# Performance work log

Measured on AMD Instinct MI355X. Metric: run time of the kernel, lower is better.

## Reference

```python
import jax, jax.numpy as jnp
import numpy as np

NUM_CLASSES = 80
N_CAND = 10  # simOTA n_candidate_k


def setup_inputs() -> dict:
    key = jax.random.key(0)
    ks = jax.random.split(key, 8)
    G, C, B = 300, NUM_CLASSES, 2
    # FPN grids for a 1280x1280 input, strides 8/16/32 -> 160^2+80^2+40^2 = 33600 anchors
    levels = [(160, 8), (80, 16), (40, 32)]
    xs, ys, ss = [], [], []
    for n, s in levels:
        yy, xx = np.meshgrid(np.arange(n), np.arange(n), indexing='ij')
        xs.append(xx.ravel()); ys.append(yy.ravel()); ss.append(np.full(n * n, s))
    x_shifts = jnp.asarray(np.concatenate(xs), jnp.float32)[None]
    y_shifts = jnp.asarray(np.concatenate(ys), jnp.float32)[None]
    strides = jnp.asarray(np.concatenate(ss), jnp.float32)
    expanded_strides = strides[None]
    A = x_shifts.shape[1]
    # gt boxes in cxcywh, image coords
    gt_cxy = jax.random.uniform(ks[0], (G, 2), jnp.float32, 0.0, 1280.0)
    gt_wh = jax.random.uniform(ks[1], (G, 2), jnp.float32, 16.0, 256.0)
    gt_bboxes_per_image = jnp.concatenate([gt_cxy, gt_wh], -1)
    gt_classes = jax.random.randint(ks[2], (G,), 0, C)
    # predicted boxes: anchor centers + noise, wh ~ a few strides
    anc_x = (x_shifts[0] + 0.5) * strides
    anc_y = (y_shifts[0] + 0.5) * strides
    pr_cxy = jnp.stack([anc_x, anc_y], -1) + jax.random.normal(ks[3], (A, 2), jnp.float32) * strides[:, None]
    pr_wh = strides[:, None] * (1.0 + 4.0 * jax.random.uniform(ks[4], (A, 2), jnp.float32))
    bboxes_preds_per_image = jnp.concatenate([pr_cxy, pr_wh], -1)
    cls_preds = jax.random.normal(ks[5], (B, A, C), jnp.float32)
    obj_preds = jax.random.normal(ks[6], (B, A, 1), jnp.float32)
    return {
        'batch_idx': 0, 'num_gt': G, 'total_num_anchors': A,
        'gt_bboxes_per_image': gt_bboxes_per_image, 'gt_classes': gt_classes,
        'bboxes_preds_per_image': bboxes_preds_per_image,
        'expanded_strides': expanded_strides, 'x_shifts': x_shifts, 'y_shifts': y_shifts,
        'cls_preds': cls_preds, 'obj_preds': obj_preds,
    }


def _pairwise_iou(gt, pr):
    # gt [G,4], pr [A,4], cxcywh -> iou [G,A] (bboxes_iou with xyxy=False)
    tl = jnp.maximum(gt[:, None, :2] - 0.5 * gt[:, None, 2:], pr[None, :, :2] - 0.5 * pr[None, :, 2:])
    br = jnp.minimum(gt[:, None, :2] + 0.5 * gt[:, None, 2:], pr[None, :, :2] + 0.5 * pr[None, :, 2:])
    wh = jnp.clip(br - tl, 0.0)
    inter = wh[..., 0] * wh[..., 1]
    area_g = gt[:, 2] * gt[:, 3]
    area_p = pr[:, 2] * pr[:, 3]
    return inter / (area_g[:, None] + area_p[None, :] - inter)


def reference(batch_idx, num_gt, total_num_anchors, gt_bboxes_per_image, gt_classes,
              bboxes_preds_per_image, expanded_strides, x_shifts, y_shifts, cls_preds, obj_preds):
    G, A = gt_bboxes_per_image.shape[0], bboxes_preds_per_image.shape[0]
    strides = expanded_strides[0]
    xc = (x_shifts[0] + 0.5) * strides  # [A] anchor centers
    yc = (y_shifts[0] + 0.5) * strides
    gx, gy, gw, gh = (gt_bboxes_per_image[:, i] for i in range(4))
    # is_in_boxes [G,A]
    in_box = ((xc[None] > (gx - 0.5 * gw)[:, None]) & ((gx + 0.5 * gw)[:, None] > xc[None]) &
              (yc[None] > (gy - 0.5 * gh)[:, None]) & ((gy + 0.5 * gh)[:, None] > yc[None]))
    r = 2.5 * strides[None]  # center_radius * stride
    in_ctr = ((xc[None] > gx[:, None] - r) & (gx[:, None] + r > xc[None]) &
              (yc[None] > gy[:, None] - r) & (gy[:, None] + r > yc[None]))
    fg_any = in_box.any(0) | in_ctr.any(0)          # fg_mask over all anchors
    candidate = in_box & in_ctr                      # is_in_boxes_and_center (full-anchor layout)
    ious = jnp.where(fg_any[None, :], _pairwise_iou(gt_bboxes_per_image, bboxes_preds_per_image), 0.0)
    # pairwise cls BCE cost; one-hot target -> factored form, never materializes [G,A,C]
    p = jnp.sqrt(jax.nn.sigmoid(cls_preds[batch_idx]) * jax.nn.sigmoid(obj_preds[batch_idx]))  # [A,C]
    p = jnp.clip(p, 1e-7, 1.0 - 1e-7)
    lp, l1p = jnp.log(p), jnp.log1p(-p)
    s_all = l1p.sum(-1)                              # [A] sum_c log(1-p_c)
    cls_loss = -((lp - l1p)[:, gt_classes].T + s_all[None, :])  # [G,A]
    # cost; 1e5 penalty for non-candidates (as in source), extra 1e6 keeps non-fg anchors
    # strictly below any fg anchor in top-k order (source only ever considers fg anchors)
    cost = cls_loss - 3.0 * jnp.log(ious + 1e-8) + 100000.0 * (~candidate) + 1000000.0 * (~fg_any)[None, :]
    # dynamic-k: sum of top-10 ious per gt, clamped to >= 1 (<= 10 inherently)
    topk_ious, _ = jax.lax.top_k(ious, N_CAND)
    dks = jnp.clip(topk_ious.sum(1).astype(jnp.int32), 1, N_CAND)  # [G]
    _, idx = jax.lax.top_k(-cost, N_CAND)            # [G,10] lowest-cost anchors per gt
    sel = (jnp.arange(N_CAND)[None, :] < dks[:, None]).astype(jnp.int32)
    matching = jnp.zeros((G, A), jnp.int32).at[jnp.arange(G)[:, None], idx].max(sel)
    # resolve anchors matched to >1 gt: keep argmax of T_scores over gts (as in source)
    multi = matching.sum(0) > 1
    best_gt = jnp.argmax(cost, axis=0)               # [A]
    matching = jnp.where(multi[None, :], (jnp.arange(G)[:, None] == best_gt[None, :]).astype(jnp.int32), matching)
    fg_final = matching.sum(0) > 0                   # final fg mask over all anchors
    num_fg = fg_final.sum()
    matched = jnp.argmax(matching, axis=0)           # [A]
    gt_matched_classes = jnp.where(fg_final, gt_classes[matched], -1)
    pred_ious = (matching.astype(ious.dtype) * ious).sum(0)  # [A], 0 where unmatched
    matched_gt_inds = jnp.where(fg_final, matched, -1)
    # fixed-shape (full-anchor) versions of the source's compacted outputs
    return (gt_matched_classes, fg_final, pred_ious, matched_gt_inds, num_fg)
```

## Files before the change

### kernel.cpp

```cpp
#include <hip/hip_runtime.h>
#include <math.h>

#define NUMC 80
#define NCAND 10
#define NK 16
#define SEGI 16
#define SEGF 16
#define FBY  8
#define GT_LDS 300

typedef unsigned long long u64;

__device__ __forceinline__ float sigmoid_stable(float x) {
    float e = expf(-fabsf(x));
    float num = (x >= 0.0f) ? 1.0f : e;
    return num / (1.0f + e);
}

__device__ __forceinline__ float s_all_for(int a, int b, int A, float so,
                                           const float* __restrict__ cls)
{
    const float4* cp4 = (const float4*)(cls + ((size_t)b * A + a) * NUMC);
    float acc = 0.0f;
    for (int q = 0; q < NUMC/4; ++q) {
        float4 v4 = cp4[q];
        float vv[4] = {v4.x, v4.y, v4.z, v4.w};
        #pragma unroll
        for (int k = 0; k < 4; ++k) {
            float sc = sigmoid_stable(vv[k]);
            float p = sqrtf(sc * so);
            p = fminf(fmaxf(p, 1e-7f), 1.0f - 1e-7f);
            acc += log1pf(-p);
        }
    }
    return acc;
}

__device__ __forceinline__ void bitonic16_desc(float (&L)[NK]) {
    #pragma unroll
    for (int j = 0; j < NK; ++j) if (!(j & 8)) { float a=L[j], b=L[j|8]; L[j]=fmaxf(a,b); L[j|8]=fminf(a,b); }
    #pragma unroll
    for (int j = 0; j < NK; ++j) if (!(j & 4)) { float a=L[j], b=L[j|4]; L[j]=fmaxf(a,b); L[j|4]=fminf(a,b); }
    #pragma unroll
    for (int j = 0; j < NK; ++j) if (!(j & 2)) { float a=L[j], b=L[j|2]; L[j]=fmaxf(a,b); L[j|2]=fminf(a,b); }
    #pragma unroll
    for (int j = 0; j < NK; ++j) if (!(j & 1)) { float a=L[j], b=L[j|1]; L[j]=fmaxf(a,b); L[j|1]=fminf(a,b); }
}

__device__ __forceinline__ void merge16_desc(float (&A_)[NK], const float (&B_)[NK]) {
    float L[NK];
    #pragma unroll
    for (int j = 0; j < NK; ++j) L[j] = fmaxf(A_[j], B_[NK-1-j]);
    bitonic16_desc(L);
    #pragma unroll
    for (int j = 0; j < NK; ++j) A_[j] = L[j];
}

struct CostRes { float cost; float iou; bool cand; };

__device__ __forceinline__ CostRes cost_od(
    int g, int a, int b, int A,
    const float* __restrict__ gt, const float4* __restrict__ pred4,
    const float4* __restrict__ anc4, const float* __restrict__ s_arr,
    const float* __restrict__ so_arr, const float* __restrict__ cls,
    const int* __restrict__ fg_any, const int* __restrict__ gcls)
{
    float gx = gt[g*4+0], gy = gt[g*4+1], gw = gt[g*4+2], gh = gt[g*4+3];
    float4 p4 = pred4[a];
    float4 an = anc4[a];
    int fga = fg_any[a];
    float px = p4.x, py = p4.y, pw = p4.z, ph = p4.w;
    float tlx = fmaxf(gx - 0.5f*gw, px - 0.5f*pw);
    float tly = fmaxf(gy - 0.5f*gh, py - 0.5f*ph);
    float brx = fminf(gx + 0.5f*gw, px + 0.5f*pw);
    float bry = fminf(gy + 0.5f*gh, py + 0.5f*ph);
    float iw = fmaxf(brx - tlx, 0.0f);
    float ih = fmaxf(bry - tly, 0.0f);
    float inter = iw * ih;
    float iou = inter / (gw*gh + pw*ph - inter);
    float fi = fga ? iou : 0.0f;
    float x = an.x, y = an.y, r = an.z;
    bool inb = (x > gx - 0.5f*gw) && (gx + 0.5f*gw > x) &&
               (y > gy - 0.5f*gh) && (gy + 0.5f*gh > y);
    bool inc = (x > gx - r) && (gx + r > x) && (y > gy - r) && (gy + r > y);
    bool cand = inb && inc;
    float so = so_arr[a];
    float cv = cls[((size_t)b * A + a) * NUMC + gcls[g]];
    float sc = sigmoid_stable(cv);
    float p = sqrtf(sc * so);
    p = fminf(fmaxf(p, 1e-7f), 1.0f - 1e-7f);
    float lp = logf(p);
    float l1p = log1pf(-p);
    float clsl = -((lp - l1p) + s_arr[a]);
    float cost = clsl - 3.0f * logf(fi + 1e-8f)
               + (cand ? 0.0f : 100000.0f)
               + (fga  ? 0.0f : 1000000.0f);
    CostRes res; res.cost = cost; res.iou = fi; res.cand = cand; return res;
}

__device__ __forceinline__ float pair_iou_masked4(
    int g, const float* __restrict__ gt, float4 p4, int fga)
{
    float gx = gt[g*4+0], gy = gt[g*4+1], gw = gt[g*4+2], gh = gt[g*4+3];
    float px = p4.x, py = p4.y, pw = p4.z, ph = p4.w;
    float tlx = fmaxf(gx - 0.5f*gw, px - 0.5f*pw);
    float tly = fmaxf(gy - 0.5f*gh, py - 0.5f*ph);
    float brx = fminf(gx + 0.5f*gw, px + 0.5f*pw);
    float bry = fminf(gy + 0.5f*gh, py + 0.5f*ph);
    float iw = fmaxf(brx - tlx, 0.0f);
    float ih = fmaxf(bry - tly, 0.0f);
    float inter = iw * ih;
    float iou = inter / (gw*gh + pw*ph - inter);
    return fga ? iou : 0.0f;
}

__global__ __launch_bounds__(512) void fused_pre_kernel(
    const int* __restrict__ bidx, int G, int A,
    const float* __restrict__ gt, const float* __restrict__ strides,
    const float* __restrict__ xs, const float* __restrict__ ys,
    const float* __restrict__ obj, const float4* __restrict__ pred4,
    float4* __restrict__ anc4, float* __restrict__ so_arr, float* __restrict__ s_arr,
    float4* __restrict__ ptlbr4, float* __restrict__ pare, float4* __restrict__ grpbox,
    int* __restrict__ fg_any, int* __restrict__ cand_any,
    int* __restrict__ count, int* __restrict__ mgt,
    int* __restrict__ mcount, int* __restrict__ fb_cnt, float* __restrict__ out)
{
    __shared__ float sgt[GT_LDS * 4];
    __shared__ float sx[64], sy[64], sr[64];
    __shared__ int   flags[512];

    int tid = threadIdx.x;
    int a0 = blockIdx.x * 64;
    int GS = (G < GT_LDS) ? G : GT_LDS;

    for (int i = tid; i < GS * 4; i += 512) sgt[i] = gt[i];
    if (tid < 64) {
        int a = a0 + tid;
        float st = 0.0f, x = 0.0f, y = 0.0f;
        if (a < A) {
            st = strides[a];
            x = (xs[a] + 0.5f) * st;
            y = (ys[a] + 0.5f) * st;
            so_arr[a] = sigmoid_stable(obj[(size_t)bidx[0] * A + a]);
        }
        sx[tid] = x; sy[tid] = y; sr[tid] = 2.5f * st;
    }
    __syncthreads();

    {
        int a_loc = tid & 63;
        int chunk = tid >> 6;
        int a = a0 + a_loc;
        int any_or = 0, any_and = 0;
        if (a < A) {
            float x = sx[a_loc], y = sy[a_loc], r = sr[a_loc];
            int gpc = (G + 7) >> 3;
            int g0 = chunk * gpc;
            int g1 = min(G, g0 + gpc);
            for (int g = g0; g < g1; ++g) {
                float gx, gy, gw, gh;
                if (g < GS) { gx = sgt[g*4+0]; gy = sgt[g*4+1]; gw = sgt[g*4+2]; gh = sgt[g*4+3]; }
                else        { gx = gt[g*4+0];  gy = gt[g*4+1];  gw = gt[g*4+2];  gh = gt[g*4+3]; }
                bool inb = (x > gx - 0.5f*gw) && (gx + 0.5f*gw > x) &&
                           (y > gy - 0.5f*gh) && (gy + 0.5f*gh > y);
                bool inc = (x > gx - r) && (gx + r > x) && (y > gy - r) && (gy + r > y);
                any_or  |= (int)(inb | inc);
                any_and |= (int)(inb && inc);
            }
        }
        flags[tid] = any_or | (any_and << 1);
    }
    __syncthreads();

    if (tid < 64) {
        int a = a0 + tid;
        float mnx = INFINITY, mny = INFINITY, mxx = -INFINITY, mxy = -INFINITY;
        if (a < A) {
            int f = flags[tid] | flags[tid+64] | flags[tid+128] | flags[tid+192]
                  | flags[tid+256] | flags[tid+320] | flags[tid+384] | flags[tid+448];
            int any = f & 1;
            fg_any[a] = any;
            cand_any[a] = (f >> 1) & 1;
            anc4[a] = make_float4(sx[tid], sy[tid], sr[tid], 0.0f);
            s_arr[a] = 0.0f;
            count[a] = 0;
            mgt[a] = -1;
            float4 p4 = pred4[a];
            pare[a] = p4.z * p4.w;
            if (any) {
                mnx = p4.x - 0.5f * p4.z;
                mny = p4.y - 0.5f * p4.w;
                mxx = p4.x + 0.5f * p4.z;
                mxy = p4.y + 0.5f * p4.w;
            }
            ptlbr4[a] = make_float4(mnx, mny, mxx, mxy);
        }
        #pragma unroll
        for (int off = 32; off > 0; off >>= 1) {
            mnx = fminf(mnx, __shfl_xor(mnx, off));
            mny = fminf(mny, __shfl_xor(mny, off));
            mxx = fmaxf(mxx, __shfl_xor(mxx, off));
            mxy = fmaxf(mxy, __shfl_xor(mxy, off));
        }
        if (tid == 0) {
            grpbox[blockIdx.x] = make_float4(mnx, mny, mxx, mxy);
            if (blockIdx.x == 0) { out[(size_t)4 * A] = 0.0f; mcount[0] = 0; fb_cnt[0] = 0; }
        }
    }
}

__global__ void sall_kernel(
    const int* __restrict__ bidx, int A,
    const float* __restrict__ cls, const float* __restrict__ so_arr,
    const int* __restrict__ cand_any, float* __restrict__ s_arr)
{
    int a = blockIdx.x * blockDim.x + threadIdx.x;
    if (a >= A) return;
    if (!cand_any[a]) return;
    s_arr[a] = s_all_for(a, bidx[0], A, so_arr[a], cls);
}

__global__ void sall_fixup_kernel(
    const int* __restrict__ bidx, int A,
    const float* __restrict__ cls, const float* __restrict__ so_arr,
    const int* __restrict__ cand_any, const int* __restrict__ fb_cnt,
    float* __restrict__ s_arr)
{
    if (fb_cnt[0] == 0) return;
    int a = blockIdx.x * blockDim.x + threadIdx.x;
    if (a >= A) return;
    if (cand_any[a]) return;
    s_arr[a] = s_all_for(a, bidx[0], A, so_arr[a], cls);
}

__global__ __launch_bounds__(64) void scanI_kernel(
    int G, int A, int seglen,
    const float* __restrict__ gt,
    const float4* __restrict__ ptlbr4, const float* __restrict__ pare,
    const float4* __restrict__ grpbox,
    float* __restrict__ piou_ws)
{
    int seg = blockIdx.x;
    int g = blockIdx.y;
    int a0 = seg * seglen;
    int a1 = min(A, a0 + seglen);
    int tid = threadIdx.x;

    float gx = gt[g*4+0], gy = gt[g*4+1], gw = gt[g*4+2], gh = gt[g*4+3];
    float gtlx = gx - 0.5f*gw, gtly = gy - 0.5f*gh;
    float gbrx = gx + 0.5f*gw, gbry = gy + 0.5f*gh;
    float ag = gw * gh;

    float ti[NK];
    #pragma unroll
    for (int j = 0; j < NK; ++j) ti[j] = 0.0f;

    for (int a = a0 + tid; a < a1; a += 64) {
        int grp = __builtin_amdgcn_readfirstlane(a >> 6);
        float4 gb = grpbox[grp];
        if ((gb.z <= gtlx) || (gb.x >= gbrx) || (gb.w <= gtly) || (gb.y >= gbry))
            continue;
        float4 p = ptlbr4[a];
        float ap = pare[a];
        float tlx = fmaxf(gtlx, p.x);
        float tly = fmaxf(gtly, p.y);
        float brx = fminf(gbrx, p.z);
        float bry = fminf(gbry, p.w);
        float iw = fmaxf(brx - tlx, 0.0f);
        float ih = fmaxf(bry - tly, 0.0f);
        float inter = iw * ih;
        float fi = inter / (ag + ap - inter);
        if (fi > ti[NK-1]) {
            ti[NK-1] = fi;
            #pragma unroll
            for (int j = NK-1; j >= 1; --j) {
                if (ti[j] > ti[j-1]) { float t = ti[j]; ti[j] = ti[j-1]; ti[j-1] = t; }
            }
        }
    }

    #pragma unroll
    for (int lv = 0; lv < 6; ++lv) {
        int off = 1 << lv;
        float pv[NK];
        #pragma unroll
        for (int j = 0; j < NK; ++j) pv[j] = __shfl_xor(ti[j], off);
        merge16_desc(ti, pv);
    }
    if (tid == 0) {
        int base = (g * SEGI + seg) * NCAND;
        #pragma unroll
        for (int j = 0; j < NCAND; ++j) piou_ws[base + j] = ti[j];
    }
}

__global__ __launch_bounds__(256) void scanC_kernel(
    const int* __restrict__ bidx, int G, int A,
    const float* __restrict__ gt, const float4* __restrict__ pred4,
    const float4* __restrict__ anc4, const float* __restrict__ s_arr,
    const float* __restrict__ so_arr, const float* __restrict__ cls,
    const int* __restrict__ fg_any, const int* __restrict__ gcls,
    const float* __restrict__ piou_ws,
    int* __restrict__ dk_arr, int* __restrict__ fb_list, int* __restrict__ fb_cnt,
    int* __restrict__ count, int* __restrict__ mgt)
{
    int g = blockIdx.x;
    int tid = threadIdx.x;
    __shared__ u64 scand[128];
    __shared__ int s_nc;
    __shared__ int s_dk;

    if (tid == 0) s_nc = 0;
    if (tid < 64) {
        float acc[NK];
        const float* ib = piou_ws + ((size_t)g * SEGI + (tid < SEGI ? tid : 0)) * NCAND;
        #pragma unroll
        for (int j = 0; j < NK; ++j)
            acc[j] = (j < NCAND && tid < SEGI) ? ib[j] : 0.0f;
        #pragma unroll
        for (int lv = 0; lv < 4; ++lv) {
            int off = 1 << lv;
            float pv[NK];
            #pragma unroll
            for (int j = 0; j < NK; ++j) pv[j] = __shfl_xor(acc[j], off);
            merge16_desc(acc, pv);
        }
        if (tid == 0) {
            float s = 0.0f;
            #pragma unroll
            for (int j = 0; j < NCAND; ++j) s += acc[j];
            int dk = (int)s;
            if (dk < 1) dk = 1;
            if (dk > NCAND) dk = NCAND;
            s_dk = dk;
            dk_arr[g] = dk;
        }
    }
    __syncthreads();

    if (tid < 243) {
        int lvl = tid / 81, slot = tid % 81, sxi = slot % 9, syi = slot / 9;
        int n, si, base;
        if (lvl == 0)      { n = 160; si = 8;  base = 0; }
        else if (lvl == 1) { n = 80;  si = 16; base = 25600; }
        else               { n = 40;  si = 32; base = 32000; }
        float sf = (float)si;
        float gx = gt[g*4+0], gy = gt[g*4+1], gw = gt[g*4+2], gh = gt[g*4+3];
        float mx = fminf(0.5f*gw, 2.5f*sf);
        float my = fminf(0.5f*gh, 2.5f*sf);
        int ilo = (int)floorf((gx - mx)/sf - 0.5f) - 1;
        int ihi = (int)ceilf ((gx + mx)/sf - 0.5f) + 1;
        int jlo = (int)floorf((gy - my)/sf - 0.5f) - 1;
        int jhi = (int)ceilf ((gy + my)/sf - 0.5f) + 1;
        if (ilo < 0) ilo = 0;
        if (jlo < 0) jlo = 0;
        if (ihi > n-1) ihi = n-1;
        if (jhi > n-1) jhi = n-1;
        int i = ilo + sxi, j = jlo + syi;
        if (i <= ihi && j <= jhi) {
            int a = base + j * n + i;
            int b = bidx[0];
            CostRes cr = cost_od(g, a, b, A, gt, pred4, anc4, s_arr, so_arr, cls, fg_any, gcls);
            if (cr.cand) {
                int k = atomicAdd(&s_nc, 1);
                if (k < 128)
                    scand[k] = ((u64)__float_as_uint(cr.cost) << 32) | (unsigned)a;
            }
        }
    }
    __syncthreads();

    if (tid == 0) {
        int nc = s_nc; if (nc > 128) nc = 128;
        int dk = s_dk;
        if (dk > nc) {
            int idx = atomicAdd(fb_cnt, 1);
            fb_list[idx] = g;
        } else {
            u64 top[NCAND];
            #pragma unroll
            for (int j = 0; j < NCAND; ++j) top[j] = ~0ULL;
            for (int t = 0; t < nc; ++t) {
                u64 v = scand[t];
                if (v < top[NCAND-1]) {
                    top[NCAND-1] = v;
                    #pragma unroll
                    for (int j = NCAND-1; j >= 1; --j) {
                        if (top[j] < top[j-1]) { u64 t2 = top[j]; top[j] = top[j-1]; top[j-1] = t2; }
                    }
                }
            }
            #pragma unroll
            for (int o = 0; o < NCAND; ++o) {
                if (o < dk) {
                    int a = (int)(top[o] & 0xffffffffULL);
                    atomicAdd(&count[a], 1);
                    atomicMax(&mgt[a], g);
                }
            }
        }
    }
}

__global__ __launch_bounds__(256) void fb_part_kernel(
    const int* __restrict__ bidx, int G, int A, int seglenF,
    const float* __restrict__ gt, const float4* __restrict__ pred4,
    const float4* __restrict__ anc4, const float* __restrict__ s_arr,
    const float* __restrict__ so_arr, const float* __restrict__ cls,
    const int* __restrict__ fg_any, const int* __restrict__ gcls,
    const int* __restrict__ fb_list, const int* __restrict__ fb_cnt,
    u64* __restrict__ fbws)
{
    __shared__ u64 s_cv[256 * NCAND];
    int nflag = fb_cnt[0];
    int tid = threadIdx.x;
    int chunk = blockIdx.x;
    int b = bidx[0];
    for (int f = blockIdx.y; f < nflag; f += FBY) {
        int g = fb_list[f];
        int a0 = chunk * seglenF;
        int a1 = min(A, a0 + seglenF);
        u64 tc[NCAND];
        #pragma unroll
        for (int j = 0; j < NCAND; ++j) tc[j] = ~0ULL;
        for (int a = a0 + tid; a < a1; a += 256) {
            CostRes cr = cost_od(g, a, b, A, gt, pred4, anc4, s_arr, so_arr, cls, fg_any, gcls);
            u64 v = ((u64)__float_as_uint(cr.cost) << 32) | (unsigned)a;
            if (v < tc[NCAND-1]) {
                tc[NCAND-1] = v;
                #pragma unroll
                for (int j = NCAND-1; j >= 1; --j) {
                    if (tc[j] < tc[j-1]) { u64 t2 = tc[j]; tc[j] = tc[j-1]; tc[j-1] = t2; }
                }
            }
        }
        #pragma unroll
        for (int j = 0; j < NCAND; ++j) s_cv[tid*NCAND+j] = tc[j];
        __syncthreads();
        for (int off = 128; off > 0; off >>= 1) {
            if (tid < off) {
                u64 rc[NCAND];
                int i = 0, k = 0;
                const u64* L = &s_cv[tid*NCAND];
                const u64* R = &s_cv[(tid+off)*NCAND];
                for (int o = 0; o < NCAND; ++o) {
                    if (L[i] < R[k]) { rc[o] = L[i]; ++i; }
                    else             { rc[o] = R[k]; ++k; }
                }
                for (int j = 0; j < NCAND; ++j) s_cv[tid*NCAND+j] = rc[j];
            }
            __syncthreads();
        }
        if (tid == 0) {
            u64* dst = fbws + ((size_t)f * SEGF + chunk) * NCAND;
            for (int j = 0; j < NCAND; ++j) dst[j] = s_cv[j];
        }
        __syncthreads();
    }
}

__global__ void fb_mark_kernel(
    const int* __restrict__ fb_list, const int* __restrict__ fb_cnt,
    const int* __restrict__ dk_arr, const u64* __restrict__ fbws,
    int* __restrict__ count, int* __restrict__ mgt)
{
    if (threadIdx.x != 0 || blockIdx.x != 0) return;
    int nflag = fb_cnt[0];
    for (int f = 0; f < nflag; ++f) {
        int g = fb_list[f];
        int dk = dk_arr[g];
        const u64* lists = fbws + (size_t)f * SEGF * NCAND;
        int p[SEGF];
        for (int q = 0; q < SEGF; ++q) p[q] = 0;
        for (int o = 0; o < dk; ++o) {
            int bs = 0; u64 bv = ~0ULL;
            for (int q = 0; q < SEGF; ++q) {
                if (p[q] < NCAND) {
                    u64 v = lists[q*NCAND + p[q]];
                    if (v < bv) { bv = v; bs = q; }
                }
            }
            p[bs]++;
            int a = (int)(bv & 0xffffffffULL);
            atomicAdd(&count[a], 1);
            atomicMax(&mgt[a], g);
        }
    }
}

__global__ void finalize_a_kernel(
    int G, int A,
    const float* __restrict__ gt, const float4* __restrict__ pred4,
    const int* __restrict__ fg_any, const int* __restrict__ gcls,
    const int* __restrict__ count, const int* __restrict__ mgt,
    int* __restrict__ mlist, int* __restrict__ mcount,
    float* __restrict__ out)
{
    int a = blockIdx.x * blockDim.x + threadIdx.x;
    if (a >= A) return;
    int cnt = count[a];
    unsigned long long m = __ballot(cnt > 0);
    if ((threadIdx.x & 63) == 0 && m) {
        atomicAdd(&out[(size_t)4*A], (float)__popcll(m));
    }
    if (cnt > 1) {
        int idx = atomicAdd(mcount, 1);
        mlist[idx] = a;
        out[(size_t)A + a] = 1.0f;
        return;
    }
    float gmc = -1.0f, mgi = -1.0f, piou = 0.0f, fg = 0.0f;
    if (cnt == 1) {
        int matched = mgt[a];
        fg = 1.0f;
        gmc = (float)gcls[matched];
        mgi = (float)matched;
        piou = pair_iou_masked4(matched, gt, pred4[a], fg_any[a]);
    }
    out[a]               = gmc;
    out[(size_t)A + a]   = fg;
    out[(size_t)2*A + a] = piou;
    out[(size_t)3*A + a] = mgi;
}

__global__ __launch_bounds__(256) void finalize_b_kernel(
    const int* __restrict__ bidx, int G, int A,
    const float* __restrict__ gt, const float4* __restrict__ pred4,
    const float4* __restrict__ anc4, const float* __restrict__ s_arr,
    const float* __restrict__ so_arr, const float* __restrict__ cls,
    const int* __restrict__ fg_any, const int* __restrict__ gcls,
    const int* __restrict__ mlist, const int* __restrict__ mcount,
    float* __restrict__ out)
{
    __shared__ float sc[256];
    __shared__ int   sg[256];
    int n = mcount[0];
    int tid = threadIdx.x;
    int b = bidx[0];
    for (int i = blockIdx.x; i < n; i += gridDim.x) {
        int a = mlist[i];
        float best = -INFINITY; int bi = 0x7fffffff;
        for (int g = tid; g < G; g += 256) {
            CostRes cr = cost_od(g, a, b, A, gt, pred4, anc4, s_arr, so_arr, cls, fg_any, gcls);
            if (cr.cost > best) { best = cr.cost; bi = g; }
        }
        sc[tid] = best; sg[tid] = bi;
        __syncthreads();
        for (int off = 128; off > 0; off >>= 1) {
            if (tid < off) {
                float c2 = sc[tid+off]; int g2 = sg[tid+off];
                if (c2 > sc[tid] || (c2 == sc[tid] && g2 < sg[tid])) { sc[tid] = c2; sg[tid] = g2; }
            }
            __syncthreads();
        }
        if (tid == 0) {
            int matched = sg[0];
            out[a]               = (float)gcls[matched];
            out[(size_t)2*A + a] = pair_iou_masked4(matched, gt, pred4[a], fg_any[a]);
            out[(size_t)3*A + a] = (float)matched;
        }
        __syncthreads();
    }
}

extern "C" void kernel_launch(void* const* d_in, const int* in_sizes, int n_in,
                              void* d_out, int out_size, void* d_ws, size_t ws_size,
                              hipStream_t stream)
{
    const int*   bidx    = (const int*)d_in[0];
    const float* gt      = (const float*)d_in[3];
    const int*   gcls    = (const int*)d_in[4];
    const float* pred    = (const float*)d_in[5];
    const float* strides = (const float*)d_in[6];
    const float* xs      = (const float*)d_in[7];
    const float* ys      = (const float*)d_in[8];
    const float* cls     = (const float*)d_in[9];
    const float* obj     = (const float*)d_in[10];
    int G = in_sizes[4];
    int A = in_sizes[6];
    float* out = (float*)d_out;
    const float4* pred4 = (const float4*)pred;

    char* ws = (char*)d_ws;
    size_t off = 0;
    auto alloc = [&](size_t bytes) -> void* {
        void* p = ws + off;
        off += (bytes + 255) & ~(size_t)255;
        return p;
    };
    int nGrp = (A + 63) / 64;
    float4* anc4     = (float4*)alloc((size_t)A * sizeof(float4));
    float*  so_arr   = (float*) alloc((size_t)A * sizeof(float));
    float*  s_arr    = (float*) alloc((size_t)A * sizeof(float));
    float4* ptlbr4   = (float4*)alloc((size_t)A * sizeof(float4));
    float*  pare     = (float*) alloc((size_t)A * sizeof(float));
    float4* grpbox   = (float4*)alloc((size_t)nGrp * sizeof(float4));
    int*    fg_any   = (int*)   alloc((size_t)A * sizeof(int));
    int*    cand_any = (int*)   alloc((size_t)A * sizeof(int));
    int*    count    = (int*)   alloc((size_t)A * sizeof(int));
    int*    mgt      = (int*)   alloc((size_t)A * sizeof(int));
    int*    mlist    = (int*)   alloc((size_t)A * sizeof(int));
    int*    mcount   = (int*)   alloc(256);
    int*    fb_cnt   = (int*)   alloc(256);
    float*  piou_ws  = (float*) alloc((size_t)G * SEGI * NCAND * sizeof(float));
    int*    dk_arr   = (int*)   alloc((size_t)G * sizeof(int));
    int*    fb_list  = (int*)   alloc((size_t)G * sizeof(int));
    u64*    fbws     = (u64*)   alloc((size_t)G * SEGF * NCAND * sizeof(u64));

    int seglenI = ((A + SEGI*64 - 1) / (SEGI*64)) * 64;
    int seglenF = ((A + SEGF*64 - 1) / (SEGF*64)) * 64;
    int blocksA256 = (A + 255) / 256;

    fused_pre_kernel<<<nGrp, 512, 0, stream>>>(
        bidx, G, A, gt, strides, xs, ys, obj, pred4,
        anc4, so_arr, s_arr, ptlbr4, pare, grpbox,
        fg_any, cand_any, count, mgt, mcount, fb_cnt, out);
    sall_kernel<<<blocksA256, 256, 0, stream>>>(
        bidx, A, cls, so_arr, cand_any, s_arr);
    scanI_kernel<<<dim3(SEGI, G), 64, 0, stream>>>(
        G, A, seglenI, gt, ptlbr4, pare, grpbox, piou_ws);
    scanC_kernel<<<G, 256, 0, stream>>>(
        bidx, G, A, gt, pred4, anc4, s_arr, so_arr, cls, fg_any, gcls,
        piou_ws, dk_arr, fb_list, fb_cnt, count, mgt);
    sall_fixup_kernel<<<blocksA256, 256, 0, stream>>>(
        bidx, A, cls, so_arr, cand_any, fb_cnt, s_arr);
    fb_part_kernel<<<dim3(SEGF, FBY), 256, 0, stream>>>(
        bidx, G, A, seglenF, gt, pred4, anc4, s_arr, so_arr, cls, fg_any, gcls,
        fb_list, fb_cnt, fbws);
    fb_mark_kernel<<<1, 64, 0, stream>>>(
        fb_list, fb_cnt, dk_arr, fbws, count, mgt);
    finalize_a_kernel<<<blocksA256, 256, 0, stream>>>(
        G, A, gt, pred4, fg_any, gcls, count, mgt, mlist, mcount, out);
    finalize_b_kernel<<<256, 256, 0, stream>>>(
        bidx, G, A, gt, pred4, anc4, s_arr, so_arr, cls, fg_any, gcls,
        mlist, mcount, out);
}
```

Before: 182.2 us.

## Fuse the simOTA kernel chain into one cooperative persistent kernel with grid syncs

Replaces the chain of nine kernel launches with a single cooperative kernel of 256 blocks that runs the phases in sequence, separated by grid-wide syncs. The per-anchor class log-sum is computed cooperatively inside the pre-pass, with eight threads per anchor writing partial terms to shared memory. The segmented top-k IoU scan and its workspace are replaced by per-gt processing inside the fused kernel, and the fallback and finalize steps now live in the same kernel with wave-level argmax reductions. This removes launch gaps and intermediate global round-trips, at the cost of grid-sync overhead and a fixed grid of 256 blocks, which limits parallelism in the per-gt phase.

Result: slower. 333.8 us (+83.2%).

```diff
diff --git a/kernel.cpp b/kernel.cpp
--- a/kernel.cpp
+++ b/kernel.cpp
@@ -1,59 +1,33 @@
 #include <hip/hip_runtime.h>
+#include <hip/hip_cooperative_groups.h>
 #include <math.h>
+
+namespace cg = cooperative_groups;
 
 #define NUMC 80
 #define NCAND 10
-#define NK 16
-#define SEGI 16
-#define SEGF 16
-#define FBY  8
+#define NB 256
+#define NT 512
 #define GT_LDS 300
 
 typedef unsigned long long u64;
+
+#define OFF_SGT 0
+#define OFF_L1P 4800
+#define OFF_FLG 25536
+#define OFF_XYR 27584
+#define OFF_IV  0
+#define OFF_SCD 20480
+#define OFF_MSC 21504
+#define OFF_CV  0
+#define OFF_ML  0
+#define OFF_MC  2048
+#define SMEM_BYTES 28352
 
 __device__ __forceinline__ float sigmoid_stable(float x) {
     float e = expf(-fabsf(x));
     float num = (x >= 0.0f) ? 1.0f : e;
     return num / (1.0f + e);
-}
-
-__device__ __forceinline__ float s_all_for(int a, int b, int A, float so,
-                                           const float* __restrict__ cls)
-{
-    const float4* cp4 = (const float4*)(cls + ((size_t)b * A + a) * NUMC);
-    float acc = 0.0f;
-    for (int q = 0; q < NUMC/4; ++q) {
-        float4 v4 = cp4[q];
-        float vv[4] = {v4.x, v4.y, v4.z, v4.w};
-        #pragma unroll
-        for (int k = 0; k < 4; ++k) {
-            float sc = sigmoid_stable(vv[k]);
-            float p = sqrtf(sc * so);
-            p = fminf(fmaxf(p, 1e-7f), 1.0f - 1e-7f);
-            acc += log1pf(-p);
-        }
-    }
-    return acc;
-}
-
-__device__ __forceinline__ void bitonic16_desc(float (&L)[NK]) {
-    #pragma unroll
-    for (int j = 0; j < NK; ++j) if (!(j & 8)) { float a=L[j], b=L[j|8]; L[j]=fmaxf(a,b); L[j|8]=fminf(a,b); }
-    #pragma unroll
-    for (int j = 0; j < NK; ++j) if (!(j & 4)) { float a=L[j], b=L[j|4]; L[j]=fmaxf(a,b); L[j|4]=fminf(a,b); }
-    #pragma unroll
-    for (int j = 0; j < NK; ++j) if (!(j & 2)) { float a=L[j], b=L[j|2]; L[j]=fmaxf(a,b); L[j|2]=fminf(a,b); }
-    #pragma unroll
-    for (int j = 0; j < NK; ++j) if (!(j & 1)) { float a=L[j], b=L[j|1]; L[j]=fmaxf(a,b); L[j|1]=fminf(a,b); }
-}
-
-__device__ __forceinline__ void merge16_desc(float (&A_)[NK], const float (&B_)[NK]) {
-    float L[NK];
-    #pragma unroll
-    for (int j = 0; j < NK; ++j) L[j] = fmaxf(A_[j], B_[NK-1-j]);
-    bitonic16_desc(L);
-    #pragma unroll
-    for (int j = 0; j < NK; ++j) A_[j] = L[j];
 }
 
 struct CostRes { float cost; float iou; bool cand; };
@@ -114,452 +88,419 @@
     return fga ? iou : 0.0f;
 }
 
-__global__ __launch_bounds__(512) void fused_pre_kernel(
+__global__ __launch_bounds__(NT, 4) void simota_all(
     const int* __restrict__ bidx, int G, int A,
-    const float* __restrict__ gt, const float* __restrict__ strides,
+    const float* __restrict__ gt, const int* __restrict__ gcls,
+    const float4* __restrict__ pred4, const float* __restrict__ strides,
     const float* __restrict__ xs, const float* __restrict__ ys,
-    const float* __restrict__ obj, const float4* __restrict__ pred4,
+    const float* __restrict__ cls, const float* __restrict__ obj,
     float4* __restrict__ anc4, float* __restrict__ so_arr, float* __restrict__ s_arr,
     float4* __restrict__ ptlbr4, float* __restrict__ pare, float4* __restrict__ grpbox,
     int* __restrict__ fg_any, int* __restrict__ cand_any,
     int* __restrict__ count, int* __restrict__ mgt,
-    int* __restrict__ mcount, int* __restrict__ fb_cnt, float* __restrict__ out)
+    int* __restrict__ dk_arr, int* __restrict__ fb_list, int* __restrict__ fb_cnt,
+    float* __restrict__ out)
 {
-    __shared__ float sgt[GT_LDS * 4];
-    __shared__ float sx[64], sy[64], sr[64];
-    __shared__ int   flags[512];
+    cg::grid_group grid = cg::this_grid();
+    __shared__ __align__(16) char smem[SMEM_BYTES];
 
     int tid = threadIdx.x;
-    int a0 = blockIdx.x * 64;
+    int bid = blockIdx.x;
+    int b = bidx[0];
     int GS = (G < GT_LDS) ? G : GT_LDS;
-
-    for (int i = tid; i < GS * 4; i += 512) sgt[i] = gt[i];
-    if (tid < 64) {
-        int a = a0 + tid;
-        float st = 0.0f, x = 0.0f, y = 0.0f;
-        if (a < A) {
-            st = strides[a];
-            x = (xs[a] + 0.5f) * st;
-            y = (ys[a] + 0.5f) * st;
-            so_arr[a] = sigmoid_stable(obj[(size_t)bidx[0] * A + a]);
-        }
-        sx[tid] = x; sy[tid] = y; sr[tid] = 2.5f * st;
+    int nGrp = (A + 63) >> 6;
+
+    {
+        float* sgt = (float*)(smem + OFF_SGT);
+        float* sl1p = (float*)(smem + OFF_L1P);
+        int*   sflg = (int*)(smem + OFF_FLG);
+        float* sx = (float*)(smem + OFF_XYR);
+        float* sy = sx + 64;
+        float* sr = sy + 64;
+
+        for (int i = tid; i < GS * 4; i += NT) sgt[i] = gt[i];
+        __syncthreads();
+
+        for (int grp = bid; grp < nGrp; grp += NB) {
+            int a0 = grp << 6;
+            if (tid < 64) {
+                int a = a0 + tid;
+                float st = 0.0f, x = 0.0f, y = 0.0f;
+                if (a < A) {
+                    st = strides[a];
+                    x = (xs[a] + 0.5f) * st;
+                    y = (ys[a] + 0.5f) * st;
+                    so_arr[a] = sigmoid_stable(obj[(size_t)b * A + a]);
+                }
+                sx[tid] = x; sy[tid] = y; sr[tid] = 2.5f * st;
+            }
+            __syncthreads();
+            {
+                int a_loc = tid & 63, chunk = tid >> 6;
+                int a = a0 + a_loc;
+                int any_or = 0, any_and = 0;
+                if (a < A) {
+                    float x = sx[a_loc], y = sy[a_loc], r = sr[a_loc];
+                    int gpc = (G + 7) >> 3;
+                    int g0 = chunk * gpc;
+                    int g1 = min(G, g0 + gpc);
+                    for (int g = g0; g < g1; ++g) {
+                        float gx, gy, gw, gh;
+                        if (g < GS) { gx = sgt[g*4+0]; gy = sgt[g*4+1]; gw = sgt[g*4+2]; gh = sgt[g*4+3]; }
+                        else        { gx = gt[g*4+0];  gy = gt[g*4+1];  gw = gt[g*4+2];  gh = gt[g*4+3]; }
+                        bool inb = (x > gx - 0.5f*gw) && (gx + 0.5f*gw > x) &&
+                                   (y > gy - 0.5f*gh) && (gy + 0.5f*gh > y);
+                        bool inc = (x > gx - r) && (gx + r > x) && (y > gy - r) && (gy + r > y);
+                        any_or  |= (int)(inb | inc);
+                        any_and |= (int)(inb && inc);
+                    }
+                }
+                sflg[tid] = any_or | (any_and << 1);
+            }
+            __syncthreads();
+            if (tid < 64) {
+                int a = a0 + tid;
+                float mnx = INFINITY, mny = INFINITY, mxx = -INFINITY, mxy = -INFINITY;
+                int f = sflg[tid] | sflg[tid+64] | sflg[tid+128] | sflg[tid+192]
+                      | sflg[tid+256] | sflg[tid+320] | sflg[tid+384] | sflg[tid+448];
+                int fg = f & 1, cd = (f >> 1) & 1;
+                if (a < A) {
+                    fg_any[a] = fg;
+                    cand_any[a] = cd;
+                    anc4[a] = make_float4(sx[tid], sy[tid], sr[tid], 0.0f);
+                    count[a] = 0;
+                    mgt[a] = -1;
+                    float4 p4 = pred4[a];
+                    pare[a] = p4.z * p4.w;
+                    if (fg) {
+                        mnx = p4.x - 0.5f * p4.z;
+                        mny = p4.y - 0.5f * p4.w;
+                        mxx = p4.x + 0.5f * p4.z;
+                        mxy = p4.y + 0.5f * p4.w;
+                    }
+                    ptlbr4[a] = make_float4(mnx, mny, mxx, mxy);
+                }
+                #pragma unroll
+                for (int off = 32; off > 0; off >>= 1) {
+                    mnx = fminf(mnx, __shfl_xor(mnx, off));
+                    mny = fminf(mny, __shfl_xor(mny, off));
+                    mxx = fmaxf(mxx, __shfl_xor(mxx, off));
+                    mxy = fmaxf(mxy, __shfl_xor(mxy, off));
+                }
+                if (tid == 0) grpbox[grp] = make_float4(mnx, mny, mxx, mxy);
+                sflg[tid] = cd;
+            }
+            __syncthreads();
+            {
+                int a_loc = tid >> 3, part = tid & 7;
+                int a = a0 + a_loc;
+                if (a < A && sflg[a_loc]) {
+                    float so = so_arr[a];
+                    const float* cp = cls + ((size_t)b * A + a) * NUMC + part * 10;
+                    #pragma unroll
+                    for (int j = 0; j < 10; ++j) {
+                        float sc = sigmoid_stable(cp[j]);
+                        float p = sqrtf(sc * so);
+                        p = fminf(fmaxf(p, 1e-7f), 1.0f - 1e-7f);
+                        sl1p[a_loc * 81 + part * 10 + j] = log1pf(-p);
+                    }
+                }
+            }
+            __syncthreads();
+            if (tid < 64) {
+                int a = a0 + tid;
+                if (a < A) {
+                    if (sflg[tid]) {
+                        float acc = 0.0f;
+                        #pragma unroll 8
+                        for (int c = 0; c < NUMC; ++c) acc += sl1p[tid * 81 + c];
+                        s_arr[a] = acc;
+                    } else {
+                        s_arr[a] = 0.0f;
+                    }
+                }
+            }
+            __syncthreads();
+        }
+        if (bid == 0 && tid == 0) { out[(size_t)4 * A] = 0.0f; fb_cnt[0] = 0; }
     }
-    __syncthreads();
+    grid.sync();
 
     {
-        int a_loc = tid & 63;
-        int chunk = tid >> 6;
-        int a = a0 + a_loc;
-        int any_or = 0, any_and = 0;
-        if (a < A) {
-            float x = sx[a_loc], y = sy[a_loc], r = sr[a_loc];
-            int gpc = (G + 7) >> 3;
-            int g0 = chunk * gpc;
-            int g1 = min(G, g0 + gpc);
-            for (int g = g0; g < g1; ++g) {
-                float gx, gy, gw, gh;
-                if (g < GS) { gx = sgt[g*4+0]; gy = sgt[g*4+1]; gw = sgt[g*4+2]; gh = sgt[g*4+3]; }
-                else        { gx = gt[g*4+0];  gy = gt[g*4+1];  gw = gt[g*4+2];  gh = gt[g*4+3]; }
-                bool inb = (x > gx - 0.5f*gw) && (gx + 0.5f*gw > x) &&
-                           (y > gy - 0.5f*gh) && (gy + 0.5f*gh > y);
-                bool inc = (x > gx - r) && (gx + r > x) && (y > gy - r) && (gy + r > y);
-                any_or  |= (int)(inb | inc);
-                any_and |= (int)(inb && inc);
-            }
-        }
-        flags[tid] = any_or | (any_and << 1);
-    }
-    __syncthreads();
-
-    if (tid < 64) {
-        int a = a0 + tid;
-        float mnx = INFINITY, mny = INFINITY, mxx = -INFINITY, mxy = -INFINITY;
-        if (a < A) {
-            int f = flags[tid] | flags[tid+64] | flags[tid+128] | flags[tid+192]
-                  | flags[tid+256] | flags[tid+320] | flags[tid+384] | flags[tid+448];
-            int any = f & 1;
-            fg_any[a] = any;
-            cand_any[a] = (f >> 1) & 1;
-            anc4[a] = make_float4(sx[tid], sy[tid], sr[tid], 0.0f);
-            s_arr[a] = 0.0f;
-            count[a] = 0;
-            mgt[a] = -1;
-            float4 p4 = pred4[a];
-            pare[a] = p4.z * p4.w;
-            if (any) {
-                mnx = p4.x - 0.5f * p4.z;
-                mny = p4.y - 0.5f * p4.w;
-                mxx = p4.x + 0.5f * p4.z;
-                mxy = p4.y + 0.5f * p4.w;
-            }
-            ptlbr4[a] = make_float4(mnx, mny, mxx, mxy);
-        }
-        #pragma unroll
-        for (int off = 32; off > 0; off >>= 1) {
-            mnx = fminf(mnx, __shfl_xor(mnx, off));
-            mny = fminf(mny, __shfl_xor(mny, off));
-            mxx = fmaxf(mxx, __shfl_xor(mxx, off));
-            mxy = fmaxf(mxy, __shfl_xor(mxy, off));
-        }
-        if (tid == 0) {
-            grpbox[blockIdx.x] = make_float4(mnx, mny, mxx, mxy);
-            if (blockIdx.x == 0) { out[(size_t)4 * A] = 0.0f; mcount[0] = 0; fb_cnt[0] = 0; }
-        }
-    }
-}
-
-__global__ void sall_kernel(
-    const int* __restrict__ bidx, int A,
-    const float* __restrict__ cls, const float* __restrict__ so_arr,
-    const int* __restrict__ cand_any, float* __restrict__ s_arr)
-{
-    int a = blockIdx.x * blockDim.x + threadIdx.x;
-    if (a >= A) return;
-    if (!cand_any[a]) return;
-    s_arr[a] = s_all_for(a, bidx[0], A, so_arr[a], cls);
-}
-
-__global__ void sall_fixup_kernel(
-    const int* __restrict__ bidx, int A,
-    const float* __restrict__ cls, const float* __restrict__ so_arr,
-    const int* __restrict__ cand_any, const int* __restrict__ fb_cnt,
-    float* __restrict__ s_arr)
-{
-    if (fb_cnt[0] == 0) return;
-    int a = blockIdx.x * blockDim.x + threadIdx.x;
-    if (a >= A) return;
-    if (cand_any[a]) return;
-    s_arr[a] = s_all_for(a, bidx[0], A, so_arr[a], cls);
-}
-
-__global__ __launch_bounds__(64) void scanI_kernel(
-    int G, int A, int seglen,
-    const float* __restrict__ gt,
-    const float4* __restrict__ ptlbr4, const float* __restrict__ pare,
-    const float4* __restrict__ grpbox,
-    float* __restrict__ piou_ws)
-{
-    int seg = blockIdx.x;
-    int g = blockIdx.y;
-    int a0 = seg * seglen;
-    int a1 = min(A, a0 + seglen);
-    int tid = threadIdx.x;
-
-    float gx = gt[g*4+0], gy = gt[g*4+1], gw = gt[g*4+2], gh = gt[g*4+3];
-    float gtlx = gx - 0.5f*gw, gtly = gy - 0.5f*gh;
-    float gbrx = gx + 0.5f*gw, gbry = gy + 0.5f*gh;
-    float ag = gw * gh;
-
-    float ti[NK];
-    #pragma unroll
-    for (int j = 0; j < NK; ++j) ti[j] = 0.0f;
-
-    for (int a = a0 + tid; a < a1; a += 64) {
-        int grp = __builtin_amdgcn_readfirstlane(a >> 6);
-        float4 gb = grpbox[grp];
-        if ((gb.z <= gtlx) || (gb.x >= gbrx) || (gb.w <= gtly) || (gb.y >= gbry))
-            continue;
-        float4 p = ptlbr4[a];
-        float ap = pare[a];
-        float tlx = fmaxf(gtlx, p.x);
-        float tly = fmaxf(gtly, p.y);
-        float brx = fminf(gbrx, p.z);
-        float bry = fminf(gbry, p.w);
-        float iw = fmaxf(brx - tlx, 0.0f);
-        float ih = fmaxf(bry - tly, 0.0f);
-        float inter = iw * ih;
-        float fi = inter / (ag + ap - inter);
-        if (fi > ti[NK-1]) {
-            ti[NK-1] = fi;
+        float* s_iv = (float*)(smem + OFF_IV);
+        u64*   scand = (u64*)(smem + OFF_SCD);
+        int*   smisc = (int*)(smem + OFF_MSC);
+
+        for (int g = bid; g < G; g += NB) {
+            float gx = gt[g*4+0], gy = gt[g*4+1], gw = gt[g*4+2], gh = gt[g*4+3];
+            float gtlx = gx - 0.5f*gw, gtly = gy - 0.5f*gh;
+            float gbrx = gx + 0.5f*gw, gbry = gy + 0.5f*gh;
+            float ag = gw * gh;
+
+            float ti[NCAND];
             #pragma unroll
-            for (int j = NK-1; j >= 1; --j) {
-                if (ti[j] > ti[j-1]) { float t = ti[j]; ti[j] = ti[j-1]; ti[j-1] = t; }
-            }
-        }
-    }
-
-    #pragma unroll
-    for (int lv = 0; lv < 6; ++lv) {
-        int off = 1 << lv;
-        float pv[NK];
-        #pragma unroll
-        for (int j = 0; j < NK; ++j) pv[j] = __shfl_xor(ti[j], off);
-        merge16_desc(ti, pv);
-    }
-    if (tid == 0) {
-        int base = (g * SEGI + seg) * NCAND;
-        #pragma unroll
-        for (int j = 0; j < NCAND; ++j) piou_ws[base + j] = ti[j];
-    }
-}
-
-__global__ __launch_bounds__(256) void scanC_kernel(
-    const int* __restrict__ bidx, int G, int A,
-    const float* __restrict__ gt, const float4* __restrict__ pred4,
-    const float4* __restrict__ anc4, const float* __restrict__ s_arr,
-    const float* __restrict__ so_arr, const float* __restrict__ cls,
-    const int* __restrict__ fg_any, const int* __restrict__ gcls,
-    const float* __restrict__ piou_ws,
-    int* __restrict__ dk_arr, int* __restrict__ fb_list, int* __restrict__ fb_cnt,
-    int* __restrict__ count, int* __restrict__ mgt)
-{
-    int g = blockIdx.x;
-    int tid = threadIdx.x;
-    __shared__ u64 scand[128];
-    __shared__ int s_nc;
-    __shared__ int s_dk;
-
-    if (tid == 0) s_nc = 0;
-    if (tid < 64) {
-        float acc[NK];
-        const float* ib = piou_ws + ((size_t)g * SEGI + (tid < SEGI ? tid : 0)) * NCAND;
-        #pragma unroll
-        for (int j = 0; j < NK; ++j)
-            acc[j] = (j < NCAND && tid < SEGI) ? ib[j] : 0.0f;
-        #pragma unroll
-        for (int lv = 0; lv < 4; ++lv) {
-            int off = 1 << lv;
-            float pv[NK];
-            #pragma unroll
-            for (int j = 0; j < NK; ++j) pv[j] = __shfl_xor(acc[j], off);
-            merge16_desc(acc, pv);
-        }
-        if (tid == 0) {
-            float s = 0.0f;
-            #pragma unroll
-            for (int j = 0; j < NCAND; ++j) s += acc[j];
-            int dk = (int)s;
-            if (dk < 1) dk = 1;
-            if (dk > NCAND) dk = NCAND;
-            s_dk = dk;
-            dk_arr[g] = dk;
-        }
-    }
-    __syncthreads();
-
-    if (tid < 243) {
-        int lvl = tid / 81, slot = tid % 81, sxi = slot % 9, syi = slot / 9;
-        int n, si, base;
-        if (lvl == 0)      { n = 160; si = 8;  base = 0; }
-        else if (lvl == 1) { n = 80;  si = 16; base = 25600; }
-        else               { n = 40;  si = 32; base = 32000; }
-        float sf = (float)si;
-        float gx = gt[g*4+0], gy = gt[g*4+1], gw = gt[g*4+2], gh = gt[g*4+3];
-        float mx = fminf(0.5f*gw, 2.5f*sf);
-        float my = fminf(0.5f*gh, 2.5f*sf);
-        int ilo = (int)floorf((gx - mx)/sf - 0.5f) - 1;
-        int ihi = (int)ceilf ((gx + mx)/sf - 0.5f) + 1;
-        int jlo = (int)floorf((gy - my)/sf - 0.5f) - 1;
-        int jhi = (int)ceilf ((gy + my)/sf - 0.5f) + 1;
-        if (ilo < 0) ilo = 0;
-        if (jlo < 0) jlo = 0;
-        if (ihi > n-1) ihi = n-1;
-        if (jhi > n-1) jhi = n-1;
-        int i = ilo + sxi, j = jlo + syi;
-        if (i <= ihi && j <= jhi) {
-            int a = base + j * n + i;
-            int b = bidx[0];
-            CostRes cr = cost_od(g, a, b, A, gt, pred4, anc4, s_arr, so_arr, cls, fg_any, gcls);
-            if (cr.cand) {
-                int k = atomicAdd(&s_nc, 1);
-                if (k < 128)
-                    scand[k] = ((u64)__float_as_uint(cr.cost) << 32) | (unsigned)a;
-            }
-        }
-    }
-    __syncthreads();
-
-    if (tid == 0) {
-        int nc = s_nc; if (nc > 128) nc = 128;
-        int dk = s_dk;
-        if (dk > nc) {
-            int idx = atomicAdd(fb_cnt, 1);
-            fb_list[idx] = g;
-        } else {
-            u64 top[NCAND];
-            #pragma unroll
-            for (int j = 0; j < NCAND; ++j) top[j] = ~0ULL;
-            for (int t = 0; t < nc; ++t) {
-                u64 v = scand[t];
-                if (v < top[NCAND-1]) {
-                    top[NCAND-1] = v;
+            for (int j = 0; j < NCAND; ++j) ti[j] = 0.0f;
+
+            for (int a = tid; a < A; a += NT) {
+                int grp = __builtin_amdgcn_readfirstlane(a >> 6);
+                float4 gb = grpbox[grp];
+                if ((gb.z <= gtlx) || (gb.x >= gbrx) || (gb.w <= gtly) || (gb.y >= gbry))
+                    continue;
+                float4 p = ptlbr4[a];
+                float ap = pare[a];
+                float tlx = fmaxf(gtlx, p.x);
+                float tly = fmaxf(gtly, p.y);
+                float brx = fminf(gbrx, p.z);
+                float bry = fminf(gbry, p.w);
+                float iw = fmaxf(brx - tlx, 0.0f);
+                float ih = fmaxf(bry - tly, 0.0f);
+                float inter = iw * ih;
+                float fi = inter / (ag + ap - inter);
+                if (fi > ti[NCAND-1]) {
+                    ti[NCAND-1] = fi;
                     #pragma unroll
                     for (int j = NCAND-1; j >= 1; --j) {
-                        if (top[j] < top[j-1]) { u64 t2 = top[j]; top[j] = top[j-1]; top[j-1] = t2; }
+                        if (ti[j] > ti[j-1]) { float t = ti[j]; ti[j] = ti[j-1]; ti[j-1] = t; }
                     }
                 }
             }
             #pragma unroll
-            for (int o = 0; o < NCAND; ++o) {
-                if (o < dk) {
-                    int a = (int)(top[o] & 0xffffffffULL);
+            for (int j = 0; j < NCAND; ++j) s_iv[tid*NCAND+j] = ti[j];
+            __syncthreads();
+            for (int off = NT/2; off > 0; off >>= 1) {
+                if (tid < off) {
+                    float ra[NCAND];
+                    int i = 0, k = 0;
+                    const float* L = &s_iv[tid*NCAND];
+                    const float* R = &s_iv[(tid+off)*NCAND];
+                    for (int o = 0; o < NCAND; ++o) {
+                        if (L[i] >= R[k]) { ra[o] = L[i]; ++i; }
+                        else              { ra[o] = R[k]; ++k; }
+                    }
+                    for (int j = 0; j < NCAND; ++j) s_iv[tid*NCAND+j] = ra[j];
+                }
+                __syncthreads();
+            }
+            if (tid == 0) {
+                float s = 0.0f;
+                #pragma unroll
+                for (int j = 0; j < NCAND; ++j) s += s_iv[j];
+                int dk = (int)s;
+                if (dk < 1) dk = 1;
+                if (dk > NCAND) dk = NCAND;
+                smisc[0] = 0;
+                smisc[1] = dk;
+                dk_arr[g] = dk;
+            }
+            __syncthreads();
+            if (tid < 243) {
+                int lvl = tid / 81, slot = tid % 81, sxi = slot % 9, syi = slot / 9;
+                int n, si, base;
+                if (lvl == 0)      { n = 160; si = 8;  base = 0; }
+                else if (lvl == 1) { n = 80;  si = 16; base = 25600; }
+                else               { n = 40;  si = 32; base = 32000; }
+                float sf = (float)si;
+                float mx = fminf(0.5f*gw, 2.5f*sf);
+                float my = fminf(0.5f*gh, 2.5f*sf);
+                int ilo = (int)floorf((gx - mx)/sf - 0.5f) - 1;
+                int ihi = (int)ceilf ((gx + mx)/sf - 0.5f) + 1;
+                int jlo = (int)floorf((gy - my)/sf - 0.5f) - 1;
+                int jhi = (int)ceilf ((gy + my)/sf - 0.5f) + 1;
+                if (ilo < 0) ilo = 0;
+                if (jlo < 0) jlo = 0;
+                if (ihi > n-1) ihi = n-1;
+                if (jhi > n-1) jhi = n-1;
+                int i = ilo + sxi, j = jlo + syi;
+                if (i <= ihi && j <= jhi) {
+                    int a = base + j * n + i;
+                    CostRes cr = cost_od(g, a, b, A, gt, pred4, anc4, s_arr, so_arr, cls, fg_any, gcls);
+                    if (cr.cand) {
+                        int k = atomicAdd(&smisc[0], 1);
+                        if (k < 128)
+                            scand[k] = ((u64)__float_as_uint(cr.cost) << 32) | (unsigned)a;
+                    }
+                }
+            }
+            __syncthreads();
+            if (tid == 0) {
+                int nc = smisc[0]; if (nc > 128) nc = 128;
+                int dk = smisc[1];
+                if (dk > nc) {
+                    int idx = atomicAdd(fb_cnt, 1);
+                    fb_list[idx] = g;
+                } else {
+                    u64 top[NCAND];
+                    #pragma unroll
+                    for (int j = 0; j < NCAND; ++j) top[j] = ~0ULL;
+                    for (int t = 0; t < nc; ++t) {
+                        u64 v = scand[t];
+                        if (v < top[NCAND-1]) {
+                            top[NCAND-1] = v;
+                            #pragma unroll
+                            for (int j = NCAND-1; j >= 1; --j) {
+                                if (top[j] < top[j-1]) { u64 t2 = top[j]; top[j] = top[j-1]; top[j-1] = t2; }
+                            }
+                        }
+                    }
+                    #pragma unroll
+                    for (int o = 0; o < NCAND; ++o) {
+                        if (o < dk) {
+                            int a = (int)(top[o] & 0xffffffffULL);
+                            atomicAdd(&count[a], 1);
+                            atomicMax(&mgt[a], g);
+                        }
+                    }
+                }
+            }
+            __syncthreads();
+        }
+    }
+    grid.sync();
+
+    int nfb = fb_cnt[0];
+    if (nfb > 0) {
+        float* sl1p = (float*)(smem + OFF_L1P);
+        int*   sflg = (int*)(smem + OFF_FLG);
+        for (int grp = bid; grp < nGrp; grp += NB) {
+            int a0 = grp << 6;
+            if (tid < 64) {
+                int a = a0 + tid;
+                sflg[tid] = (a < A) ? cand_any[a] : 1;
+            }
+            __syncthreads();
+            {
+                int a_loc = tid >> 3, part = tid & 7;
+                int a = a0 + a_loc;
+                if (a < A && !sflg[a_loc]) {
+                    float so = so_arr[a];
+                    const float* cp = cls + ((size_t)b * A + a) * NUMC + part * 10;
+                    #pragma unroll
+                    for (int j = 0; j < 10; ++j) {
+                        float sc = sigmoid_stable(cp[j]);
+                        float p = sqrtf(sc * so);
+                        p = fminf(fmaxf(p, 1e-7f), 1.0f - 1e-7f);
+                        sl1p[a_loc * 81 + part * 10 + j] = log1pf(-p);
+                    }
+                }
+            }
+            __syncthreads();
+            if (tid < 64) {
+                int a = a0 + tid;
+                if (a < A && !sflg[tid]) {
+                    float acc = 0.0f;
+                    #pragma unroll 8
+                    for (int c = 0; c < NUMC; ++c) acc += sl1p[tid * 81 + c];
+                    s_arr[a] = acc;
+                }
+            }
+            __syncthreads();
+        }
+    }
+    grid.sync();
+
+    if (nfb > 0) {
+        u64* s_cv = (u64*)(smem + OFF_CV);
+        for (int f = bid; f < nfb; f += NB) {
+            int g = fb_list[f];
+            int dk = dk_arr[g];
+            if (tid < 256) {
+                u64 tc[NCAND];
+                #pragma unroll
+                for (int j = 0; j < NCAND; ++j) tc[j] = ~0ULL;
+                for (int a = tid; a < A; a += 256) {
+                    CostRes cr = cost_od(g, a, b, A, gt, pred4, anc4, s_arr, so_arr, cls, fg_any, gcls);
+                    u64 v = ((u64)__float_as_uint(cr.cost) << 32) | (unsigned)a;
+                    if (v < tc[NCAND-1]) {
+                        tc[NCAND-1] = v;
+                        #pragma unroll
+                        for (int j = NCAND-1; j >= 1; --j) {
+                            if (tc[j] < tc[j-1]) { u64 t2 = tc[j]; tc[j] = tc[j-1]; tc[j-1] = t2; }
+                        }
+                    }
+                }
+                #pragma unroll
+                for (int j = 0; j < NCAND; ++j) s_cv[tid*NCAND+j] = tc[j];
+            }
+            __syncthreads();
+            for (int off = 128; off > 0; off >>= 1) {
+                if (tid < off) {
+                    u64 rc[NCAND];
+                    int i = 0, k = 0;
+                    const u64* L = &s_cv[tid*NCAND];
+                    const u64* R = &s_cv[(tid+off)*NCAND];
+                    for (int o = 0; o < NCAND; ++o) {
+                        if (L[i] < R[k]) { rc[o] = L[i]; ++i; }
+                        else             { rc[o] = R[k]; ++k; }
+                    }
+                    for (int j = 0; j < NCAND; ++j) s_cv[tid*NCAND+j] = rc[j];
+                }
+                __syncthreads();
+            }
+            if (tid == 0) {
+                for (int o = 0; o < dk; ++o) {
+                    int a = (int)(s_cv[o] & 0xffffffffULL);
                     atomicAdd(&count[a], 1);
                     atomicMax(&mgt[a], g);
                 }
             }
+            __syncthreads();
         }
     }
-}
-
-__global__ __launch_bounds__(256) void fb_part_kernel(
-    const int* __restrict__ bidx, int G, int A, int seglenF,
-    const float* __restrict__ gt, const float4* __restrict__ pred4,
-    const float4* __restrict__ anc4, const float* __restrict__ s_arr,
-    const float* __restrict__ so_arr, const float* __restrict__ cls,
-    const int* __restrict__ fg_any, const int* __restrict__ gcls,
-    const int* __restrict__ fb_list, const int* __restrict__ fb_cnt,
-    u64* __restrict__ fbws)
-{
-    __shared__ u64 s_cv[256 * NCAND];
-    int nflag = fb_cnt[0];
-    int tid = threadIdx.x;
-    int chunk = blockIdx.x;
-    int b = bidx[0];
-    for (int f = blockIdx.y; f < nflag; f += FBY) {
-        int g = fb_list[f];
-        int a0 = chunk * seglenF;
-        int a1 = min(A, a0 + seglenF);
-        u64 tc[NCAND];
-        #pragma unroll
-        for (int j = 0; j < NCAND; ++j) tc[j] = ~0ULL;
-        for (int a = a0 + tid; a < a1; a += 256) {
-            CostRes cr = cost_od(g, a, b, A, gt, pred4, anc4, s_arr, so_arr, cls, fg_any, gcls);
-            u64 v = ((u64)__float_as_uint(cr.cost) << 32) | (unsigned)a;
-            if (v < tc[NCAND-1]) {
-                tc[NCAND-1] = v;
-                #pragma unroll
-                for (int j = NCAND-1; j >= 1; --j) {
-                    if (tc[j] < tc[j-1]) { u64 t2 = tc[j]; tc[j] = tc[j-1]; tc[j-1] = t2; }
-                }
-            }
-        }
-        #pragma unroll
-        for (int j = 0; j < NCAND; ++j) s_cv[tid*NCAND+j] = tc[j];
+    grid.sync();
+
+    {
+        int* mlist = (int*)(smem + OFF_ML);
+        int* mcnt  = (int*)(smem + OFF_MC);
+        if (tid == 0) mcnt[0] = 0;
         __syncthreads();
-        for (int off = 128; off > 0; off >>= 1) {
-            if (tid < off) {
-                u64 rc[NCAND];
-                int i = 0, k = 0;
-                const u64* L = &s_cv[tid*NCAND];
-                const u64* R = &s_cv[(tid+off)*NCAND];
-                for (int o = 0; o < NCAND; ++o) {
-                    if (L[i] < R[k]) { rc[o] = L[i]; ++i; }
-                    else             { rc[o] = R[k]; ++k; }
-                }
-                for (int j = 0; j < NCAND; ++j) s_cv[tid*NCAND+j] = rc[j];
-            }
-            __syncthreads();
-        }
-        if (tid == 0) {
-            u64* dst = fbws + ((size_t)f * SEGF + chunk) * NCAND;
-            for (int j = 0; j < NCAND; ++j) dst[j] = s_cv[j];
+        int a = bid * NT + tid;
+        int cnt = (a < A) ? count[a] : 0;
+        unsigned long long m = __ballot(cnt > 0);
+        if ((tid & 63) == 0 && m) {
+            atomicAdd(&out[(size_t)4*A], (float)__popcll(m));
+        }
+        if (a < A) {
+            if (cnt > 1) {
+                int k = atomicAdd(mcnt, 1);
+                mlist[k] = a;
+                out[(size_t)A + a] = 1.0f;
+            } else {
+                float gmc = -1.0f, mgi = -1.0f, piou = 0.0f, fg = 0.0f;
+                if (cnt == 1) {
+                    int matched = mgt[a];
+                    fg = 1.0f;
+                    gmc = (float)gcls[matched];
+                    mgi = (float)matched;
+                    piou = pair_iou_masked4(matched, gt, pred4[a], fg_any[a]);
+                }
+                out[a]               = gmc;
+                out[(size_t)A + a]   = fg;
+                out[(size_t)2*A + a] = piou;
+                out[(size_t)3*A + a] = mgi;
+            }
         }
         __syncthreads();
-    }
-}
-
-__global__ void fb_mark_kernel(
-    const int* __restrict__ fb_list, const int* __restrict__ fb_cnt,
-    const int* __restrict__ dk_arr, const u64* __restrict__ fbws,
-    int* __restrict__ count, int* __restrict__ mgt)
-{
-    if (threadIdx.x != 0 || blockIdx.x != 0) return;
-    int nflag = fb_cnt[0];
-    for (int f = 0; f < nflag; ++f) {
-        int g = fb_list[f];
-        int dk = dk_arr[g];
-        const u64* lists = fbws + (size_t)f * SEGF * NCAND;
-        int p[SEGF];
-        for (int q = 0; q < SEGF; ++q) p[q] = 0;
-        for (int o = 0; o < dk; ++o) {
-            int bs = 0; u64 bv = ~0ULL;
-            for (int q = 0; q < SEGF; ++q) {
-                if (p[q] < NCAND) {
-                    u64 v = lists[q*NCAND + p[q]];
-                    if (v < bv) { bv = v; bs = q; }
-                }
-            }
-            p[bs]++;
-            int a = (int)(bv & 0xffffffffULL);
-            atomicAdd(&count[a], 1);
-            atomicMax(&mgt[a], g);
-        }
-    }
-}
-
-__global__ void finalize_a_kernel(
-    int G, int A,
-    const float* __restrict__ gt, const float4* __restrict__ pred4,
-    const int* __restrict__ fg_any, const int* __restrict__ gcls,
-    const int* __restrict__ count, const int* __restrict__ mgt,
-    int* __restrict__ mlist, int* __restrict__ mcount,
-    float* __restrict__ out)
-{
-    int a = blockIdx.x * blockDim.x + threadIdx.x;
-    if (a >= A) return;
-    int cnt = count[a];
-    unsigned long long m = __ballot(cnt > 0);
-    if ((threadIdx.x & 63) == 0 && m) {
-        atomicAdd(&out[(size_t)4*A], (float)__popcll(m));
-    }
-    if (cnt > 1) {
-        int idx = atomicAdd(mcount, 1);
-        mlist[idx] = a;
-        out[(size_t)A + a] = 1.0f;
-        return;
-    }
-    float gmc = -1.0f, mgi = -1.0f, piou = 0.0f, fg = 0.0f;
-    if (cnt == 1) {
-        int matched = mgt[a];
-        fg = 1.0f;
-        gmc = (float)gcls[matched];
-        mgi = (float)matched;
-        piou = pair_iou_masked4(matched, gt, pred4[a], fg_any[a]);
-    }
-    out[a]               = gmc;
-    out[(size_t)A + a]   = fg;
-    out[(size_t)2*A + a] = piou;
-    out[(size_t)3*A + a] = mgi;
-}
-
-__global__ __launch_bounds__(256) void finalize_b_kernel(
-    const int* __restrict__ bidx, int G, int A,
-    const float* __restrict__ gt, const float4* __restrict__ pred4,
-    const float4* __restrict__ anc4, const float* __restrict__ s_arr,
-    const float* __restrict__ so_arr, const float* __restrict__ cls,
-    const int* __restrict__ fg_any, const int* __restrict__ gcls,
-    const int* __restrict__ mlist, const int* __restrict__ mcount,
-    float* __restrict__ out)
-{
-    __shared__ float sc[256];
-    __shared__ int   sg[256];
-    int n = mcount[0];
-    int tid = threadIdx.x;
-    int b = bidx[0];
-    for (int i = blockIdx.x; i < n; i += gridDim.x) {
-        int a = mlist[i];
-        float best = -INFINITY; int bi = 0x7fffffff;
-        for (int g = tid; g < G; g += 256) {
-            CostRes cr = cost_od(g, a, b, A, gt, pred4, anc4, s_arr, so_arr, cls, fg_any, gcls);
-            if (cr.cost > best) { best = cr.cost; bi = g; }
-        }
-        sc[tid] = best; sg[tid] = bi;
-        __syncthreads();
-        for (int off = 128; off > 0; off >>= 1) {
-            if (tid < off) {
-                float c2 = sc[tid+off]; int g2 = sg[tid+off];
-                if (c2 > sc[tid] || (c2 == sc[tid] && g2 < sg[tid])) { sc[tid] = c2; sg[tid] = g2; }
-            }
-            __syncthreads();
-        }
-        if (tid == 0) {
-            int matched = sg[0];
-            out[a]               = (float)gcls[matched];
-            out[(size_t)2*A + a] = pair_iou_masked4(matched, gt, pred4[a], fg_any[a]);
-            out[(size_t)3*A + a] = (float)matched;
-        }
-        __syncthreads();
+        int nm = mcnt[0];
+        int wid = tid >> 6, lane = tid & 63;
+        for (int i = wid; i < nm; i += 8) {
+            int aa = mlist[i];
+            float best = -INFINITY; int bi = 0x7fffffff;
+            for (int gg = lane; gg < G; gg += 64) {
+                CostRes cr = cost_od(gg, aa, b, A, gt, pred4, anc4, s_arr, so_arr, cls, fg_any, gcls);
+                if (cr.cost > best) { best = cr.cost; bi = gg; }
+            }
+            #pragma unroll
+            for (int off = 32; off > 0; off >>= 1) {
+                float ob = __shfl_xor(best, off);
+                int obi = __shfl_xor(bi, off);
+                if (ob > best || (ob == best && obi < bi)) { best = ob; bi = obi; }
+            }
+            if (lane == 0) {
+                out[aa]               = (float)gcls[bi];
+                out[(size_t)2*A + aa] = pair_iou_masked4(bi, gt, pred4[aa], fg_any[aa]);
+                out[(size_t)3*A + aa] = (float)bi;
+            }
+        }
     }
 }
 
@@ -599,39 +540,17 @@
     int*    cand_any = (int*)   alloc((size_t)A * sizeof(int));
     int*    count    = (int*)   alloc((size_t)A * sizeof(int));
     int*    mgt      = (int*)   alloc((size_t)A * sizeof(int));
-    int*    mlist    = (int*)   alloc((size_t)A * sizeof(int));
-    int*    mcount   = (int*)   alloc(256);
-    int*    fb_cnt   = (int*)   alloc(256);
-    float*  piou_ws  = (float*) alloc((size_t)G * SEGI * NCAND * sizeof(float));
     int*    dk_arr   = (int*)   alloc((size_t)G * sizeof(int));
     int*    fb_list  = (int*)   alloc((size_t)G * sizeof(int));
-    u64*    fbws     = (u64*)   alloc((size_t)G * SEGF * NCAND * sizeof(u64));
-
-    int seglenI = ((A + SEGI*64 - 1) / (SEGI*64)) * 64;
-    int seglenF = ((A + SEGF*64 - 1) / (SEGF*64)) * 64;
-    int blocksA256 = (A + 255) / 256;
-
-    fused_pre_kernel<<<nGrp, 512, 0, stream>>>(
-        bidx, G, A, gt, strides, xs, ys, obj, pred4,
-        anc4, so_arr, s_arr, ptlbr4, pare, grpbox,
-        fg_any, cand_any, count, mgt, mcount, fb_cnt, out);
-    sall_kernel<<<blocksA256, 256, 0, stream>>>(
-        bidx, A, cls, so_arr, cand_any, s_arr);
-    scanI_kernel<<<dim3(SEGI, G), 64, 0, stream>>>(
-        G, A, seglenI, gt, ptlbr4, pare, grpbox, piou_ws);
-    scanC_kernel<<<G, 256, 0, stream>>>(
-        bidx, G, A, gt, pred4, anc4, s_arr, so_arr, cls, fg_any, gcls,
-        piou_ws, dk_arr, fb_list, fb_cnt, count, mgt);
-    sall_fixup_kernel<<<blocksA256, 256, 0, stream>>>(
-        bidx, A, cls, so_arr, cand_any, fb_cnt, s_arr);
-    fb_part_kernel<<<dim3(SEGF, FBY), 256, 0, stream>>>(
-        bidx, G, A, seglenF, gt, pred4, anc4, s_arr, so_arr, cls, fg_any, gcls,
-        fb_list, fb_cnt, fbws);
-    fb_mark_kernel<<<1, 64, 0, stream>>>(
-        fb_list, fb_cnt, dk_arr, fbws, count, mgt);
-    finalize_a_kernel<<<blocksA256, 256, 0, stream>>>(
-        G, A, gt, pred4, fg_any, gcls, count, mgt, mlist, mcount, out);
-    finalize_b_kernel<<<256, 256, 0, stream>>>(
-        bidx, G, A, gt, pred4, anc4, s_arr, so_arr, cls, fg_any, gcls,
-        mlist, mcount, out);
+    int*    fb_cnt   = (int*)   alloc(256);
+
+    void* kargs[] = {
+        (void*)&bidx, (void*)&G, (void*)&A, (void*)&gt, (void*)&gcls, (void*)&pred4,
+        (void*)&strides, (void*)&xs, (void*)&ys, (void*)&cls, (void*)&obj,
+        (void*)&anc4, (void*)&so_arr, (void*)&s_arr, (void*)&ptlbr4, (void*)&pare,
+        (void*)&grpbox, (void*)&fg_any, (void*)&cand_any, (void*)&count, (void*)&mgt,
+        (void*)&dk_arr, (void*)&fb_list, (void*)&fb_cnt, (void*)&out
+    };
+    hipLaunchCooperativeKernel((const void*)simota_all, dim3(NB), dim3(NT),
+                               kargs, 0, stream);
 }
```
